# Optimization experiments

Measured on AMD Instinct MI355X. Metric: run time of the kernel, lower is better.

Reference implementation:

```python
import jax, jax.numpy as jnp
import numpy as np

B, N, K, C, NH = 2, 16384, 16, 256, 4
HD = C // NH  # head_dim = 64


def knn_gather(feat, idx):
    # feat: [B, N, D], idx: [B, N, K] -> [B, N, K, D]
    b, n, k = idx.shape
    d = feat.shape[-1]
    flat = jnp.take_along_axis(feat, idx.reshape(b, n * k)[..., None], axis=1)
    return flat.reshape(b, n, k, d)


def setup_inputs() -> dict:
    key = jax.random.key(0)
    ks = jax.random.split(key, 16)
    s_c = 1.0 / np.sqrt(C)
    s_4 = 1.0 / np.sqrt(4.0)
    s_hd = 1.0 / np.sqrt(HD)
    return {
        'h': jax.random.normal(ks[0], (B, N, C), jnp.float32),
        'P': jax.random.normal(ks[1], (B, 3, N), jnp.float32),
        'idx': jax.random.randint(ks[2], (B, N, K), 0, N),
        'Wq': jax.random.normal(ks[3], (C, C), jnp.float32) * s_c,
        'Wk': jax.random.normal(ks[4], (C, C), jnp.float32) * s_c,
        'Wv': jax.random.normal(ks[5], (C, C), jnp.float32) * s_c,
        'Wp1': jax.random.normal(ks[6], (4, C), jnp.float32) * s_4,
        'bp1': jnp.zeros((C,), jnp.float32),
        'Wp2': jax.random.normal(ks[7], (C, C), jnp.float32) * s_c,
        'bp2': jnp.zeros((C,), jnp.float32),
        'Wa1': jax.random.normal(ks[8], (HD, HD), jnp.float32) * s_hd,
        'ba1': jnp.zeros((HD,), jnp.float32),
        'Wa2': jax.random.normal(ks[9], (HD, 1), jnp.float32) * s_hd,
        'ba2': jnp.zeros((1,), jnp.float32),
        'Wo': jax.random.normal(ks[10], (C, C), jnp.float32) * s_c,
        'bo': jnp.zeros((C,), jnp.float32),
    }


def reference(h, P, idx, Wq, Wk, Wv, Wp1, bp1, Wp2, bp2, Wa1, ba1, Wa2, ba2, Wo, bo):
    b, n, c = h.shape
    P_t = jnp.swapaxes(P, 1, 2)                       # [B, N, 3]
    P_nbr = knn_gather(P_t, idx)                      # [B, N, K, 3]
    rel_pos = P_nbr - P_t[:, :, None, :]              # [B, N, K, 3]
    dist = jnp.linalg.norm(rel_pos, axis=-1, keepdims=True)
    geom = jnp.concatenate([rel_pos, dist], axis=-1)  # [B, N, K, 4]
    pe = jax.nn.relu(geom @ Wp1 + bp1) @ Wp2 + bp2    # [B, N, K, C]
    pe = pe.reshape(b, n, K, NH, HD)

    Q = (h @ Wq).reshape(b, n, 1, NH, HD)
    K_nbr = knn_gather(h @ Wk, idx).reshape(b, n, K, NH, HD)
    V_nbr = knn_gather(h @ Wv, idx).reshape(b, n, K, NH, HD)

    relation = Q - K_nbr + pe                          # [B, N, K, NH, HD]
    logits = jax.nn.relu(relation @ Wa1 + ba1) @ Wa2 + ba2  # [B, N, K, NH, 1]
    attn = jax.nn.softmax(logits, axis=2)              # softmax over K
    agg = jnp.sum(attn * (V_nbr + pe), axis=2)         # [B, N, NH, HD]
    agg = agg.reshape(b, n, c)
    return agg @ Wo + bo
```

## Files before the change

kernel.cpp:

```cpp
#include <hip/hip_runtime.h>
#include <hip/hip_bf16.h>

#define BB 2
#define NN 16384
#define KK 16
#define CC 256
#define NHH 4
#define HDD 64
#define BN (BB*NN)
#define HP 260

typedef __attribute__((ext_vector_type(8))) short short8;
typedef __attribute__((ext_vector_type(4))) short s4;
typedef __attribute__((ext_vector_type(4))) float f32x4;

__device__ __forceinline__ float bf2f(unsigned short u) {
    union { unsigned u32; float f; } x; x.u32 = ((unsigned)u) << 16; return x.f;
}
__device__ __forceinline__ unsigned short f2bf(float f) {
    union { float f; unsigned u; } x; x.f = f;
    unsigned r = x.u + 0x7FFFu + ((x.u >> 16) & 1u);
    return (unsigned short)(r >> 16);
}
__device__ __forceinline__ short8 ld8_lds(const unsigned short* p) {
    s4 lo = *(const s4*)(p);
    s4 hi = *(const s4*)(p + 4);
    short8 r;
    r[0] = lo[0]; r[1] = lo[1]; r[2] = lo[2]; r[3] = lo[3];
    r[4] = hi[0]; r[5] = hi[1]; r[6] = hi[2]; r[7] = hi[3];
    return r;
}

__global__ __launch_bounds__(256) void prep_kernel(
    const float* __restrict__ Wq, const float* __restrict__ Wk,
    const float* __restrict__ Wv, const float* __restrict__ Wp2,
    const float* __restrict__ Wo, const float* __restrict__ Wa1,
    const float* __restrict__ bp2, const float* __restrict__ ba1,
    const float* __restrict__ Wp1,
    unsigned short* WqaT, unsigned short* WkaT, unsigned short* WvT,
    unsigned short* WpeaT, unsigned short* Wp2T, unsigned short* WoT,
    float* b_u, unsigned short* Wp1aT)
{
    const int z = blockIdx.y;
    const int t = threadIdx.x;
    if (z < 3) {
        const float* W = (z == 0) ? Wq : (z == 1) ? Wk : Wp2;
        unsigned short* out = (z == 0) ? WqaT : (z == 1) ? WkaT : WpeaT;
        const int k = blockIdx.x;
        __shared__ float wrow[CC];
        __shared__ float a1[HDD * HDD];
        wrow[t] = W[k * CC + t];
        for (int i = t; i < HDD * HDD; i += 256) a1[i] = Wa1[i];
        __syncthreads();
        const int c = t;
        const int h0 = c & ~63;
        const int cl = c & 63;
        float s = 0.f;
        #pragma unroll 8
        for (int j = 0; j < HDD; ++j) s += wrow[h0 + j] * a1[j * HDD + cl];
        out[c * CC + k] = f2bf(s);
    } else if (z < 6) {
        const float* W = (z == 3) ? Wv : (z == 4) ? Wp2 : Wo;
        unsigned short* out = (z == 3) ? WvT : (z == 4) ? Wp2T : WoT;
        const int k = blockIdx.x;
        out[t * CC + k] = f2bf(W[k * CC + t]);
    } else {
        if (blockIdx.x == 0) {
            __shared__ float a1[HDD * HDD];
            for (int i = t; i < HDD * HDD; i += 256) a1[i] = Wa1[i];
            __syncthreads();
            const int c = t;
            const int h0 = c & ~63;
            const int cl = c & 63;
            float s = ba1[cl];
            #pragma unroll 8
            for (int j = 0; j < HDD; ++j) s += bp2[h0 + j] * a1[j * HDD + cl];
            b_u[c] = s;
        } else if (blockIdx.x == 1) {
            const int c = t;
            #pragma unroll
            for (int j = 0; j < 8; ++j)
                Wp1aT[c * 8 + j] = (j < 4) ? f2bf(Wp1[j * CC + c]) : (unsigned short)0;
        }
    }
}

__global__ __launch_bounds__(256) void h2bf_kernel(const float* __restrict__ h,
                                                   unsigned short* __restrict__ hbf)
{
    const int i = blockIdx.x * blockDim.x + threadIdx.x;
    const float4 v = ((const float4*)h)[i];
    ushort4 o;
    o.x = f2bf(v.x); o.y = f2bf(v.y); o.z = f2bf(v.z); o.w = f2bf(v.w);
    ((ushort4*)hbf)[i] = o;
}

template<bool FINAL>
__global__ __launch_bounds__(256) void gemm64_kernel(
    const unsigned short* __restrict__ A,
    const unsigned short* __restrict__ BT0, const unsigned short* __restrict__ BT1,
    const unsigned short* __restrict__ BT2,
    unsigned short* D0, unsigned short* D1, unsigned short* D2,
    float* Dout, const float* __restrict__ bias)
{
    const int m0 = blockIdx.x * 64;
    const unsigned short* BT;
    unsigned short* Dst = nullptr;
    if (!FINAL) {
        const int z = blockIdx.y;
        BT  = (z == 0) ? BT0 : (z == 1) ? BT1 : BT2;
        Dst = (z == 0) ? D0  : (z == 1) ? D1  : D2;
    } else {
        BT = BT0;
    }

    __shared__ __align__(16) unsigned short As[64 * 264];
    const int t = threadIdx.x;
    #pragma unroll
    for (int i = 0; i < 8; ++i) {
        const int flat = i * 2048 + t * 8;
        const int r = flat >> 8, c = flat & 255;
        short8 v = *(const short8*)(A + (size_t)(m0 + r) * CC + c);
        *(short8*)(&As[r * 264 + c]) = v;
    }
    __syncthreads();

    const int lane = t & 63, w = t >> 6;
    const int lr = lane & 15, lg = lane >> 4;

    f32x4 acc[4][4];
    #pragma unroll
    for (int mi = 0; mi < 4; ++mi)
        #pragma unroll
        for (int ni = 0; ni < 4; ++ni) acc[mi][ni] = (f32x4){0.f, 0.f, 0.f, 0.f};

    #pragma unroll
    for (int kk = 0; kk < 8; ++kk) {
        const int ko = kk * 32 + lg * 8;
        short8 a[4];
        #pragma unroll
        for (int mi = 0; mi < 4; ++mi)
            a[mi] = *(const short8*)(&As[(mi * 16 + lr) * 264 + ko]);
        #pragma unroll
        for (int ni = 0; ni < 4; ++ni) {
            const int col = w * 64 + ni * 16 + lr;
            short8 b = *(const short8*)(BT + (size_t)col * CC + ko);
            #pragma unroll
            for (int mi = 0; mi < 4; ++mi)
                acc[mi][ni] = __builtin_amdgcn_mfma_f32_16x16x32_bf16(a[mi], b, acc[mi][ni], 0, 0, 0);
        }
    }

    #pragma unroll
    for (int mi = 0; mi < 4; ++mi) {
        #pragma unroll
        for (int ni = 0; ni < 4; ++ni) {
            const int col = w * 64 + ni * 16 + lr;
            #pragma unroll
            for (int reg = 0; reg < 4; ++reg) {
                const int row = m0 + mi * 16 + lg * 4 + reg;
                const float v = acc[mi][ni][reg];
                if (FINAL) Dout[(size_t)row * CC + col] = v + bias[col];
                else       Dst[(size_t)row * CC + col] = f2bf(v);
            }
        }
    }
}

__global__ __launch_bounds__(256, 4) void fused_attn_kernel(
    const float* __restrict__ P, const int* __restrict__ idx,
    const unsigned short* __restrict__ Wp1aT, const float* __restrict__ bp1,
    const float* __restrict__ Wa2, const float* __restrict__ bp2,
    const unsigned short* __restrict__ QAbf, const unsigned short* __restrict__ KAbf,
    const unsigned short* __restrict__ Vbf,  const unsigned short* __restrict__ WpeaT,
    const unsigned short* __restrict__ Wp2T, const float* __restrict__ b_u,
    unsigned short* __restrict__ aggbf)
{
    const int pt0 = blockIdx.x * 4;
    const int b = pt0 >> 14;
    const int n0 = pt0 & (NN - 1);
    const int t = threadIdx.x;
    const int lane = t & 63, w = t >> 6;
    const int lr = lane & 15, lg = lane >> 4;

    __shared__ int nbrL[64];
    __shared__ __align__(16) unsigned short geomP[64 * 8];
    __shared__ __align__(16) unsigned short hidL[64 * HP];
    __shared__ __align__(16) unsigned short attnA[16 * 72];
    __shared__ unsigned short vbarL[16 * 72];

    const short8 zero8 = {0, 0, 0, 0, 0, 0, 0, 0};

    float qab[4][4];
    float wa2v[4], bp1v[4];
    #pragma unroll
    for (int ni = 0; ni < 4; ++ni) {
        const int c = w * 64 + ni * 16 + lr;
        wa2v[ni] = Wa2[ni * 16 + lr];
        bp1v[ni] = bp1[c];
        const float bu = b_u[c];
        #pragma unroll
        for (int mi = 0; mi < 4; ++mi)
            qab[mi][ni] = bf2f(QAbf[(size_t)(pt0 + mi) * CC + c]) + bu;
    }

    for (int i = t; i < 576; i += 256) ((unsigned*)attnA)[i] = 0;
    if (t < 64) {
        const int g = t >> 4, k = t & 15;
        const int nb = idx[(size_t)(pt0 + g) * KK + k];
        nbrL[t] = nb;
        const float* Pb = P + (size_t)b * 3 * NN;
        const int nc = n0 + g;
        const float rx = Pb[nb] - Pb[nc];
        const float ry = Pb[NN + nb] - Pb[NN + nc];
        const float rz = Pb[2 * NN + nb] - Pb[2 * NN + nc];
        const float d = sqrtf(rx * rx + ry * ry + rz * rz);
        short8 gp = {(short)f2bf(rx), (short)f2bf(ry), (short)f2bf(rz), (short)f2bf(d),
                     0, 0, 0, 0};
        *(short8*)(&geomP[t * 8]) = gp;
    }
    __syncthreads();

    {
        short8 bb[4];
        #pragma unroll
        for (int ni = 0; ni < 4; ++ni) {
            const int col = w * 64 + ni * 16 + lr;
            bb[ni] = (lg == 0) ? *(const short8*)(Wp1aT + col * 8) : zero8;
        }
        #pragma unroll
        for (int mi = 0; mi < 4; ++mi) {
            short8 ag = (lg == 0) ? *(const short8*)(&geomP[(mi * 16 + lr) * 8]) : zero8;
            #pragma unroll
            for (int ni = 0; ni < 4; ++ni) {
                f32x4 ah = (f32x4){bp1v[ni], bp1v[ni], bp1v[ni], bp1v[ni]};
                ah = __builtin_amdgcn_mfma_f32_16x16x32_bf16(ag, bb[ni], ah, 0, 0, 0);
                const int col = w * 64 + ni * 16 + lr;
                #pragma unroll
                for (int reg = 0; reg < 4; ++reg)
                    hidL[(mi * 16 + lg * 4 + reg) * HP + col] = f2bf(fmaxf(ah[reg], 0.f));
            }
        }
    }
    __syncthreads();

    f32x4 acc[4][4];
    #pragma unroll
    for (int mi = 0; mi < 4; ++mi)
        #pragma unroll
        for (int ni = 0; ni < 4; ++ni) {
            const float v = qab[mi][ni];
            acc[mi][ni] = (f32x4){v, v, v, v};
        }

    #pragma unroll
    for (int kk = 0; kk < 8; ++kk) {
        const int ko = kk * 32 + lg * 8;
        short8 a[4];
        #pragma unroll
        for (int mi = 0; mi < 4; ++mi)
            a[mi] = ld8_lds(&hidL[(mi * 16 + lr) * HP + ko]);
        #pragma unroll
        for (int ni = 0; ni < 4; ++ni) {
            const int col = w * 64 + ni * 16 + lr;
            short8 bfr = *(const short8*)(WpeaT + (size_t)col * CC + ko);
            #pragma unroll
            for (int mi = 0; mi < 4; ++mi)
                acc[mi][ni] = __builtin_amdgcn_mfma_f32_16x16x32_bf16(a[mi], bfr, acc[mi][ni], 0, 0, 0);
        }
    }

    #pragma unroll
    for (int mi = 0; mi < 4; ++mi) {
        unsigned short ka[4][4];
        #pragma unroll
        for (int reg = 0; reg < 4; ++reg) {
            const int r = mi * 16 + lg * 4 + reg;
            const size_t base = ((size_t)b * NN + nbrL[r]) * CC;
            #pragma unroll
            for (int ni = 0; ni < 4; ++ni)
                ka[reg][ni] = KAbf[base + w * 64 + ni * 16 + lr];
        }
        float pl[4];
        #pragma unroll
        for (int reg = 0; reg < 4; ++reg) {
            float s = 0.f;
            #pragma unroll
            for (int ni = 0; ni < 4; ++ni) {
                const float u = acc[mi][ni][reg] - bf2f(ka[reg][ni]);
                s += fmaxf(u, 0.f) * wa2v[ni];
            }
            s += __shfl_xor(s, 1);
            s += __shfl_xor(s, 2);
            s += __shfl_xor(s, 4);
            s += __shfl_xor(s, 8);
            pl[reg] = s;
        }
        float m = fmaxf(fmaxf(pl[0], pl[1]), fmaxf(pl[2], pl[3]));
        m = fmaxf(m, __shfl_xor(m, 16));
        m = fmaxf(m, __shfl_xor(m, 32));
        float e[4], s = 0.f;
        #pragma unroll
        for (int reg = 0; reg < 4; ++reg) { e[reg] = __expf(pl[reg] - m); s += e[reg]; }
        s += __shfl_xor(s, 16);
        s += __shfl_xor(s, 32);
        const float inv = 1.f / s;
        if (lr == 0) {
            #pragma unroll
            for (int reg = 0; reg < 4; ++reg)
                attnA[(mi * 4 + w) * 72 + mi * 16 + lg * 4 + reg] = f2bf(e[reg] * inv);
        }
    }
    __syncthreads();

    unsigned short vv[4][16];
    #pragma unroll
    for (int i = 0; i < 4; ++i) {
        const int gh = w * 4 + i;
        const int g = gh >> 2, hh = gh & 3;
        #pragma unroll
        for (int k = 0; k < 16; ++k) {
            const int r = g * 16 + k;
            vv[i][k] = Vbf[((size_t)b * NN + nbrL[r]) * CC + hh * 64 + lane];
        }
    }

    #pragma unroll
    for (int ni = 0; ni < 4; ++ni) {
        const int colAbs = w * 64 + ni * 16 + lr;
        f32x4 ab = (f32x4){0.f, 0.f, 0.f, 0.f};
        #pragma unroll
        for (int kk = 0; kk < 2; ++kk) {
            short8 aa = ld8_lds(&attnA[lr * 72 + kk * 32 + lg * 8]);
            short8 hb;
            #pragma unroll
            for (int j = 0; j < 8; ++j)
                hb[j] = (short)hidL[(kk * 32 + lg * 8 + j) * HP + colAbs];
            ab = __builtin_amdgcn_mfma_f32_16x16x32_bf16(aa, hb, ab, 0, 0, 0);
        }
        #pragma unroll
        for (int reg = 0; reg < 4; ++reg)
            hidL[(lg * 4 + reg) * HP + colAbs] = f2bf(ab[reg]);
    }

    {
        #pragma unroll
        for (int i = 0; i < 4; ++i) {
            const int gh = w * 4 + i;
            const int g = gh >> 2;
            float s = 0.f;
            #pragma unroll
            for (int k = 0; k < 16; ++k)
                s += bf2f(attnA[gh * 72 + g * 16 + k]) * bf2f(vv[i][k]);
            vbarL[gh * 72 + lane] = f2bf(s);
        }
    }
    __syncthreads();

    f32x4 acc2[4];
    #pragma unroll
    for (int ni = 0; ni < 4; ++ni) acc2[ni] = (f32x4){0.f, 0.f, 0.f, 0.f};
    #pragma unroll
    for (int kk = 0; kk < 8; ++kk) {
        const int ko = kk * 32 + lg * 8;
        short8 a = ld8_lds(&hidL[lr * HP + ko]);
        #pragma unroll
        for (int ni = 0; ni < 4; ++ni) {
            const int col = w * 64 + ni * 16 + lr;
            short8 bfr = *(const short8*)(Wp2T + (size_t)col * CC + ko);
            acc2[ni] = __builtin_amdgcn_mfma_f32_16x16x32_bf16(a, bfr, acc2[ni], 0, 0, 0);
        }
    }
    #pragma unroll
    for (int ni = 0; ni < 4; ++ni) {
        const int cl = ni * 16 + lr;
        const int c = w * 64 + cl;
        float pv;
        if      (w == 0) pv = acc2[ni][0];
        else if (w == 1) pv = acc2[ni][1];
        else if (w == 2) pv = acc2[ni][2];
        else             pv = acc2[ni][3];
        const float v = pv + bf2f(vbarL[(lg * 4 + w) * 72 + cl]) + bp2[c];
        aggbf[(size_t)(pt0 + lg) * CC + c] = f2bf(v);
    }
}

extern "C" void kernel_launch(void* const* d_in, const int* in_sizes, int n_in,
                              void* d_out, int out_size, void* d_ws, size_t ws_size,
                              hipStream_t stream)
{
    const float* h   = (const float*)d_in[0];
    const float* P   = (const float*)d_in[1];
    const int*   idx = (const int*)d_in[2];
    const float* Wq  = (const float*)d_in[3];
    const float* Wk  = (const float*)d_in[4];
    const float* Wv  = (const float*)d_in[5];
    const float* Wp1 = (const float*)d_in[6];
    const float* bp1 = (const float*)d_in[7];
    const float* Wp2 = (const float*)d_in[8];
    const float* bp2 = (const float*)d_in[9];
    const float* Wa1 = (const float*)d_in[10];
    const float* ba1 = (const float*)d_in[11];
    const float* Wa2 = (const float*)d_in[12];
    const float* Wo  = (const float*)d_in[14];
    const float* bo  = (const float*)d_in[15];

    char* ws = (char*)d_ws;
    const size_t MB16 = 16777216;
    unsigned short* WqaT  = (unsigned short*)(ws + 0);
    unsigned short* WkaT  = (unsigned short*)(ws + 131072);
    unsigned short* WvT   = (unsigned short*)(ws + 262144);
    unsigned short* WpeaT = (unsigned short*)(ws + 393216);
    unsigned short* Wp2T  = (unsigned short*)(ws + 524288);
    unsigned short* WoT   = (unsigned short*)(ws + 655360);
    float*          b_u   = (float*)(ws + 786432);
    unsigned short* Wp1aT = (unsigned short*)(ws + 787456);
    const size_t base = 1 << 20;
    unsigned short* hbf   = (unsigned short*)(ws + base + 0 * MB16);
    unsigned short* QAbf  = (unsigned short*)(ws + base + 1 * MB16);
    unsigned short* KAbf  = (unsigned short*)(ws + base + 2 * MB16);
    unsigned short* Vbf   = (unsigned short*)(ws + base + 3 * MB16);
    unsigned short* aggbf = (unsigned short*)(ws + base + 4 * MB16);
    if (ws_size < base + 5 * MB16) return;

    prep_kernel<<<dim3(256, 7), 256, 0, stream>>>(Wq, Wk, Wv, Wp2, Wo, Wa1, bp2, ba1, Wp1,
                                                  WqaT, WkaT, WvT, WpeaT, Wp2T, WoT,
                                                  b_u, Wp1aT);
    h2bf_kernel<<<BN * CC / 4 / 256, 256, 0, stream>>>(h, hbf);
    gemm64_kernel<false><<<dim3(BN / 64, 3), 256, 0, stream>>>(
        hbf, WqaT, WkaT, WvT, QAbf, KAbf, Vbf, nullptr, nullptr);
    fused_attn_kernel<<<BN / 4, 256, 0, stream>>>(P, idx, Wp1aT, bp1, Wa2, bp2,
                                                  QAbf, KAbf, Vbf, WpeaT, Wp2T, b_u, aggbf);
    gemm64_kernel<true><<<dim3(BN / 64, 1), 256, 0, stream>>>(
        aggbf, WoT, nullptr, nullptr, nullptr, nullptr, nullptr, (float*)d_out, bo);
}
```

Measured before the change: 395.8 us.

## Transpose pe MFMA so gathers are vectorized ushort4 and fold bias into Q GEMM

The positional-encoding GEMM in the attention kernel is transposed (weights as the A operand, hidden as B), so each lane holds four consecutive channels. This allows K/Q neighbour rows and V rows to be gathered as 8-byte ushort4 loads instead of scalar 2-byte loads. The softmax reduction is reorganised to match the new lane mapping. The b_u bias is now added in the Q projection GEMM epilogue rather than inside the attention kernel. The risks are a different register pressure profile and an unchanged MFMA count.

```diff
diff --git a/kernel.cpp b/kernel.cpp
--- a/kernel.cpp
+++ b/kernel.cpp
@@ -106,8 +106,9 @@
     const int m0 = blockIdx.x * 64;
     const unsigned short* BT;
     unsigned short* Dst = nullptr;
+    int z = 0;
     if (!FINAL) {
-        const int z = blockIdx.y;
+        z = blockIdx.y;
         BT  = (z == 0) ? BT0 : (z == 1) ? BT1 : BT2;
         Dst = (z == 0) ? D0  : (z == 1) ? D1  : D2;
     } else {
@@ -156,12 +157,13 @@
         #pragma unroll
         for (int ni = 0; ni < 4; ++ni) {
             const int col = w * 64 + ni * 16 + lr;
+            const float bc = (FINAL || z == 0) ? bias[col] : 0.f;
             #pragma unroll
             for (int reg = 0; reg < 4; ++reg) {
                 const int row = m0 + mi * 16 + lg * 4 + reg;
                 const float v = acc[mi][ni][reg];
                 if (FINAL) Dout[(size_t)row * CC + col] = v + bias[col];
-                else       Dst[(size_t)row * CC + col] = f2bf(v);
+                else       Dst[(size_t)row * CC + col] = f2bf(v + bc);
             }
         }
     }
@@ -173,7 +175,7 @@
     const float* __restrict__ Wa2, const float* __restrict__ bp2,
     const unsigned short* __restrict__ QAbf, const unsigned short* __restrict__ KAbf,
     const unsigned short* __restrict__ Vbf,  const unsigned short* __restrict__ WpeaT,
-    const unsigned short* __restrict__ Wp2T, const float* __restrict__ b_u,
+    const unsigned short* __restrict__ Wp2T,
     unsigned short* __restrict__ aggbf)
 {
     const int pt0 = blockIdx.x * 4;
@@ -191,18 +193,9 @@
 
     const short8 zero8 = {0, 0, 0, 0, 0, 0, 0, 0};
 
-    float qab[4][4];
-    float wa2v[4], bp1v[4];
-    #pragma unroll
-    for (int ni = 0; ni < 4; ++ni) {
-        const int c = w * 64 + ni * 16 + lr;
-        wa2v[ni] = Wa2[ni * 16 + lr];
-        bp1v[ni] = bp1[c];
-        const float bu = b_u[c];
-        #pragma unroll
-        for (int mi = 0; mi < 4; ++mi)
-            qab[mi][ni] = bf2f(QAbf[(size_t)(pt0 + mi) * CC + c]) + bu;
-    }
+    float bp1v[4];
+    #pragma unroll
+    for (int ni = 0; ni < 4; ++ni) bp1v[ni] = bp1[w * 64 + ni * 16 + lr];
 
     for (int i = t; i < 576; i += 256) ((unsigned*)attnA)[i] = 0;
     if (t < 64) {
@@ -244,86 +237,88 @@
     }
     __syncthreads();
 
-    f32x4 acc[4][4];
-    #pragma unroll
-    for (int mi = 0; mi < 4; ++mi)
-        #pragma unroll
-        for (int ni = 0; ni < 4; ++ni) {
-            const float v = qab[mi][ni];
-            acc[mi][ni] = (f32x4){v, v, v, v};
-        }
-
-    #pragma unroll
-    for (int kk = 0; kk < 8; ++kk) {
-        const int ko = kk * 32 + lg * 8;
-        short8 a[4];
-        #pragma unroll
-        for (int mi = 0; mi < 4; ++mi)
-            a[mi] = ld8_lds(&hidL[(mi * 16 + lr) * HP + ko]);
-        #pragma unroll
-        for (int ni = 0; ni < 4; ++ni) {
-            const int col = w * 64 + ni * 16 + lr;
-            short8 bfr = *(const short8*)(WpeaT + (size_t)col * CC + ko);
-            #pragma unroll
-            for (int mi = 0; mi < 4; ++mi)
-                acc[mi][ni] = __builtin_amdgcn_mfma_f32_16x16x32_bf16(a[mi], bfr, acc[mi][ni], 0, 0, 0);
-        }
-    }
-
-    #pragma unroll
-    for (int mi = 0; mi < 4; ++mi) {
-        unsigned short ka[4][4];
-        #pragma unroll
-        for (int reg = 0; reg < 4; ++reg) {
-            const int r = mi * 16 + lg * 4 + reg;
-            const size_t base = ((size_t)b * NN + nbrL[r]) * CC;
-            #pragma unroll
-            for (int ni = 0; ni < 4; ++ni)
-                ka[reg][ni] = KAbf[base + w * 64 + ni * 16 + lr];
-        }
-        float pl[4];
-        #pragma unroll
-        for (int reg = 0; reg < 4; ++reg) {
-            float s = 0.f;
-            #pragma unroll
-            for (int ni = 0; ni < 4; ++ni) {
-                const float u = acc[mi][ni][reg] - bf2f(ka[reg][ni]);
-                s += fmaxf(u, 0.f) * wa2v[ni];
+    const size_t bNN = (size_t)b * NN;
+    int nb4[4];
+    #pragma unroll
+    for (int RB = 0; RB < 4; ++RB) nb4[RB] = nbrL[RB * 16 + lr];
+
+    f32x4 slog[4];
+    #pragma unroll
+    for (int RB = 0; RB < 4; ++RB) slog[RB] = (f32x4){0.f, 0.f, 0.f, 0.f};
+
+    #pragma unroll
+    for (int pair = 0; pair < 2; ++pair) {
+        ushort4 kaP[2][4], qaP[2][4];
+        #pragma unroll
+        for (int cbi = 0; cbi < 2; ++cbi) {
+            const int CB = pair * 2 + cbi;
+            const int cb0 = w * 64 + CB * 16 + lg * 4;
+            #pragma unroll
+            for (int RB = 0; RB < 4; ++RB) {
+                kaP[cbi][RB] = *(const ushort4*)(KAbf + (bNN + nb4[RB]) * CC + cb0);
+                qaP[cbi][RB] = *(const ushort4*)(QAbf + (size_t)(pt0 + RB) * CC + cb0);
             }
-            s += __shfl_xor(s, 1);
-            s += __shfl_xor(s, 2);
-            s += __shfl_xor(s, 4);
-            s += __shfl_xor(s, 8);
-            pl[reg] = s;
-        }
-        float m = fmaxf(fmaxf(pl[0], pl[1]), fmaxf(pl[2], pl[3]));
-        m = fmaxf(m, __shfl_xor(m, 16));
-        m = fmaxf(m, __shfl_xor(m, 32));
-        float e[4], s = 0.f;
-        #pragma unroll
-        for (int reg = 0; reg < 4; ++reg) { e[reg] = __expf(pl[reg] - m); s += e[reg]; }
+        }
+
+        f32x4 acc8[2][4];
+        #pragma unroll
+        for (int cbi = 0; cbi < 2; ++cbi)
+            #pragma unroll
+            for (int RB = 0; RB < 4; ++RB) acc8[cbi][RB] = (f32x4){0.f, 0.f, 0.f, 0.f};
+
+        #pragma unroll
+        for (int kk = 0; kk < 8; ++kk) {
+            const int ko = kk * 32 + lg * 8;
+            short8 aw0 = *(const short8*)(WpeaT + (size_t)(w * 64 + (pair * 2 + 0) * 16 + lr) * CC + ko);
+            short8 aw1 = *(const short8*)(WpeaT + (size_t)(w * 64 + (pair * 2 + 1) * 16 + lr) * CC + ko);
+            #pragma unroll
+            for (int RB = 0; RB < 4; ++RB) {
+                short8 bh = ld8_lds(&hidL[(RB * 16 + lr) * HP + ko]);
+                acc8[0][RB] = __builtin_amdgcn_mfma_f32_16x16x32_bf16(aw0, bh, acc8[0][RB], 0, 0, 0);
+                acc8[1][RB] = __builtin_amdgcn_mfma_f32_16x16x32_bf16(aw1, bh, acc8[1][RB], 0, 0, 0);
+            }
+        }
+
+        #pragma unroll
+        for (int cbi = 0; cbi < 2; ++cbi) {
+            const int CB = pair * 2 + cbi;
+            const float4 w4 = *(const float4*)(Wa2 + CB * 16 + lg * 4);
+            #pragma unroll
+            for (int RB = 0; RB < 4; ++RB) {
+                const ushort4 ka4 = kaP[cbi][RB], qa4 = qaP[cbi][RB];
+                slog[RB][0] += fmaxf(acc8[cbi][RB][0] + bf2f(qa4.x) - bf2f(ka4.x), 0.f) * w4.x;
+                slog[RB][1] += fmaxf(acc8[cbi][RB][1] + bf2f(qa4.y) - bf2f(ka4.y), 0.f) * w4.y;
+                slog[RB][2] += fmaxf(acc8[cbi][RB][2] + bf2f(qa4.z) - bf2f(ka4.z), 0.f) * w4.z;
+                slog[RB][3] += fmaxf(acc8[cbi][RB][3] + bf2f(qa4.w) - bf2f(ka4.w), 0.f) * w4.w;
+            }
+        }
+    }
+
+    #pragma unroll
+    for (int RB = 0; RB < 4; ++RB) {
+        float s = slog[RB][0] + slog[RB][1] + slog[RB][2] + slog[RB][3];
         s += __shfl_xor(s, 16);
         s += __shfl_xor(s, 32);
-        const float inv = 1.f / s;
-        if (lr == 0) {
-            #pragma unroll
-            for (int reg = 0; reg < 4; ++reg)
-                attnA[(mi * 4 + w) * 72 + mi * 16 + lg * 4 + reg] = f2bf(e[reg] * inv);
-        }
+        float m = s;
+        m = fmaxf(m, __shfl_xor(m, 1));
+        m = fmaxf(m, __shfl_xor(m, 2));
+        m = fmaxf(m, __shfl_xor(m, 4));
+        m = fmaxf(m, __shfl_xor(m, 8));
+        const float e = __expf(s - m);
+        float d = e;
+        d += __shfl_xor(d, 1);
+        d += __shfl_xor(d, 2);
+        d += __shfl_xor(d, 4);
+        d += __shfl_xor(d, 8);
+        if (lg == 0)
+            attnA[(RB * 4 + w) * 72 + RB * 16 + lr] = f2bf(e / d);
     }
     __syncthreads();
 
-    unsigned short vv[4][16];
-    #pragma unroll
-    for (int i = 0; i < 4; ++i) {
-        const int gh = w * 4 + i;
-        const int g = gh >> 2, hh = gh & 3;
-        #pragma unroll
-        for (int k = 0; k < 16; ++k) {
-            const int r = g * 16 + k;
-            vv[i][k] = Vbf[((size_t)b * NN + nbrL[r]) * CC + hh * 64 + lane];
-        }
-    }
+    ushort4 vv[16];
+    #pragma unroll
+    for (int k = 0; k < 16; ++k)
+        vv[k] = *(const ushort4*)(Vbf + (bNN + nbrL[w * 16 + k]) * CC + lane * 4);
 
     #pragma unroll
     for (int ni = 0; ni < 4; ++ni) {
@@ -344,16 +339,20 @@
     }
 
     {
-        #pragma unroll
-        for (int i = 0; i < 4; ++i) {
-            const int gh = w * 4 + i;
-            const int g = gh >> 2;
-            float s = 0.f;
-            #pragma unroll
-            for (int k = 0; k < 16; ++k)
-                s += bf2f(attnA[gh * 72 + g * 16 + k]) * bf2f(vv[i][k]);
-            vbarL[gh * 72 + lane] = f2bf(s);
-        }
+        const int hh = lane >> 4;
+        const int dbase = (lane & 15) * 4;
+        float s0 = 0.f, s1 = 0.f, s2 = 0.f, s3 = 0.f;
+        #pragma unroll
+        for (int k = 0; k < 16; ++k) {
+            const float at = bf2f(attnA[(w * 4 + hh) * 72 + w * 16 + k]);
+            s0 += at * bf2f((unsigned short)vv[k].x);
+            s1 += at * bf2f((unsigned short)vv[k].y);
+            s2 += at * bf2f((unsigned short)vv[k].z);
+            s3 += at * bf2f((unsigned short)vv[k].w);
+        }
+        ushort4 o;
+        o.x = f2bf(s0); o.y = f2bf(s1); o.z = f2bf(s2); o.w = f2bf(s3);
+        *(ushort4*)(&vbarL[(w * 4 + hh) * 72 + dbase]) = o;
     }
     __syncthreads();
 
@@ -428,9 +427,9 @@
                                                   b_u, Wp1aT);
     h2bf_kernel<<<BN * CC / 4 / 256, 256, 0, stream>>>(h, hbf);
     gemm64_kernel<false><<<dim3(BN / 64, 3), 256, 0, stream>>>(
-        hbf, WqaT, WkaT, WvT, QAbf, KAbf, Vbf, nullptr, nullptr);
+        hbf, WqaT, WkaT, WvT, QAbf, KAbf, Vbf, nullptr, b_u);
     fused_attn_kernel<<<BN / 4, 256, 0, stream>>>(P, idx, Wp1aT, bp1, Wa2, bp2,
-                                                  QAbf, KAbf, Vbf, WpeaT, Wp2T, b_u, aggbf);
+                                                  QAbf, KAbf, Vbf, WpeaT, Wp2T, aggbf);
     gemm64_kernel<true><<<dim3(BN / 64, 1), 256, 0, stream>>>(
         aggbf, WoT, nullptr, nullptr, nullptr, nullptr, nullptr, (float*)d_out, bo);
 }
```

Result: slower. 420.0 us (+6.1%).

## Fold query bias into GEMM, per-wave geometry MFMA, vectorized V gather

Applied to the files above, without the earlier changes.

The b_u bias is now added in the QKV GEMM epilogue for the Q output, so the attention kernel no longer loads and adds it. Each wave now computes the geometry features for its own point in registers and runs the first position-encoding MFMA directly, which removes the geomP LDS staging buffer and one block barrier. The V neighbour gather now loads ushort4 vectors per lane instead of scalar shorts, and the attention-weighted V sum works on four channels per lane. Launch bounds drop from 4 to 3 blocks per CU, which gives the compiler more registers but may lower occupancy.

```diff
diff --git a/kernel.cpp b/kernel.cpp
--- a/kernel.cpp
+++ b/kernel.cpp
@@ -106,8 +106,9 @@
     const int m0 = blockIdx.x * 64;
     const unsigned short* BT;
     unsigned short* Dst = nullptr;
+    int z = 0;
     if (!FINAL) {
-        const int z = blockIdx.y;
+        z = blockIdx.y;
         BT  = (z == 0) ? BT0 : (z == 1) ? BT1 : BT2;
         Dst = (z == 0) ? D0  : (z == 1) ? D1  : D2;
     } else {
@@ -156,24 +157,25 @@
         #pragma unroll
         for (int ni = 0; ni < 4; ++ni) {
             const int col = w * 64 + ni * 16 + lr;
+            const float bc = (FINAL || z == 0) ? bias[col] : 0.f;
             #pragma unroll
             for (int reg = 0; reg < 4; ++reg) {
                 const int row = m0 + mi * 16 + lg * 4 + reg;
                 const float v = acc[mi][ni][reg];
                 if (FINAL) Dout[(size_t)row * CC + col] = v + bias[col];
-                else       Dst[(size_t)row * CC + col] = f2bf(v);
+                else       Dst[(size_t)row * CC + col] = f2bf(v + bc);
             }
         }
     }
 }
 
-__global__ __launch_bounds__(256, 4) void fused_attn_kernel(
+__global__ __launch_bounds__(256, 3) void fused_attn_kernel(
     const float* __restrict__ P, const int* __restrict__ idx,
     const unsigned short* __restrict__ Wp1aT, const float* __restrict__ bp1,
     const float* __restrict__ Wa2, const float* __restrict__ bp2,
     const unsigned short* __restrict__ QAbf, const unsigned short* __restrict__ KAbf,
     const unsigned short* __restrict__ Vbf,  const unsigned short* __restrict__ WpeaT,
-    const unsigned short* __restrict__ Wp2T, const float* __restrict__ b_u,
+    const unsigned short* __restrict__ Wp2T,
     unsigned short* __restrict__ aggbf)
 {
     const int pt0 = blockIdx.x * 4;
@@ -184,7 +186,6 @@
     const int lr = lane & 15, lg = lane >> 4;
 
     __shared__ int nbrL[64];
-    __shared__ __align__(16) unsigned short geomP[64 * 8];
     __shared__ __align__(16) unsigned short hidL[64 * HP];
     __shared__ __align__(16) unsigned short attnA[16 * 72];
     __shared__ unsigned short vbarL[16 * 72];
@@ -192,55 +193,43 @@
     const short8 zero8 = {0, 0, 0, 0, 0, 0, 0, 0};
 
     float qab[4][4];
-    float wa2v[4], bp1v[4];
+    float wa2v[4];
     #pragma unroll
     for (int ni = 0; ni < 4; ++ni) {
         const int c = w * 64 + ni * 16 + lr;
         wa2v[ni] = Wa2[ni * 16 + lr];
-        bp1v[ni] = bp1[c];
-        const float bu = b_u[c];
         #pragma unroll
         for (int mi = 0; mi < 4; ++mi)
-            qab[mi][ni] = bf2f(QAbf[(size_t)(pt0 + mi) * CC + c]) + bu;
+            qab[mi][ni] = bf2f(QAbf[(size_t)(pt0 + mi) * CC + c]);
     }
 
     for (int i = t; i < 576; i += 256) ((unsigned*)attnA)[i] = 0;
-    if (t < 64) {
-        const int g = t >> 4, k = t & 15;
-        const int nb = idx[(size_t)(pt0 + g) * KK + k];
-        nbrL[t] = nb;
+
+    float rx = 0.f, ry = 0.f, rz = 0.f, dd = 0.f;
+    if (lane < 16) {
+        const int nb_ = idx[(size_t)(pt0 + w) * KK + lane];
+        nbrL[w * 16 + lane] = nb_;
         const float* Pb = P + (size_t)b * 3 * NN;
-        const int nc = n0 + g;
-        const float rx = Pb[nb] - Pb[nc];
-        const float ry = Pb[NN + nb] - Pb[NN + nc];
-        const float rz = Pb[2 * NN + nb] - Pb[2 * NN + nc];
-        const float d = sqrtf(rx * rx + ry * ry + rz * rz);
-        short8 gp = {(short)f2bf(rx), (short)f2bf(ry), (short)f2bf(rz), (short)f2bf(d),
-                     0, 0, 0, 0};
-        *(short8*)(&geomP[t * 8]) = gp;
-    }
-    __syncthreads();
-
-    {
-        short8 bb[4];
-        #pragma unroll
-        for (int ni = 0; ni < 4; ++ni) {
-            const int col = w * 64 + ni * 16 + lr;
-            bb[ni] = (lg == 0) ? *(const short8*)(Wp1aT + col * 8) : zero8;
-        }
-        #pragma unroll
-        for (int mi = 0; mi < 4; ++mi) {
-            short8 ag = (lg == 0) ? *(const short8*)(&geomP[(mi * 16 + lr) * 8]) : zero8;
-            #pragma unroll
-            for (int ni = 0; ni < 4; ++ni) {
-                f32x4 ah = (f32x4){bp1v[ni], bp1v[ni], bp1v[ni], bp1v[ni]};
-                ah = __builtin_amdgcn_mfma_f32_16x16x32_bf16(ag, bb[ni], ah, 0, 0, 0);
-                const int col = w * 64 + ni * 16 + lr;
-                #pragma unroll
-                for (int reg = 0; reg < 4; ++reg)
-                    hidL[(mi * 16 + lg * 4 + reg) * HP + col] = f2bf(fmaxf(ah[reg], 0.f));
-            }
-        }
+        const int nc = n0 + w;
+        rx = Pb[nb_] - Pb[nc];
+        ry = Pb[NN + nb_] - Pb[NN + nc];
+        rz = Pb[2 * NN + nb_] - Pb[2 * NN + nc];
+        dd = sqrtf(rx * rx + ry * ry + rz * rz);
+    }
+    short8 ag = zero8;
+    if (lane < 16) {
+        ag[0] = (short)f2bf(rx); ag[1] = (short)f2bf(ry);
+        ag[2] = (short)f2bf(rz); ag[3] = (short)f2bf(dd);
+    }
+    #pragma unroll
+    for (int nb = 0; nb < 16; ++nb) {
+        short8 bb = (lg == 0) ? *(const short8*)(Wp1aT + (nb * 16 + lr) * 8) : zero8;
+        const float bp = bp1[nb * 16 + lr];
+        f32x4 ah = (f32x4){bp, bp, bp, bp};
+        ah = __builtin_amdgcn_mfma_f32_16x16x32_bf16(ag, bb, ah, 0, 0, 0);
+        #pragma unroll
+        for (int reg = 0; reg < 4; ++reg)
+            hidL[(w * 16 + lg * 4 + reg) * HP + nb * 16 + lr] = f2bf(fmaxf(ah[reg], 0.f));
     }
     __syncthreads();
 
@@ -313,17 +302,11 @@
     }
     __syncthreads();
 
-    unsigned short vv[4][16];
-    #pragma unroll
-    for (int i = 0; i < 4; ++i) {
-        const int gh = w * 4 + i;
-        const int g = gh >> 2, hh = gh & 3;
-        #pragma unroll
-        for (int k = 0; k < 16; ++k) {
-            const int r = g * 16 + k;
-            vv[i][k] = Vbf[((size_t)b * NN + nbrL[r]) * CC + hh * 64 + lane];
-        }
-    }
+    const size_t bNN = (size_t)b * NN;
+    ushort4 vv[16];
+    #pragma unroll
+    for (int k = 0; k < 16; ++k)
+        vv[k] = *(const ushort4*)(Vbf + (bNN + nbrL[w * 16 + k]) * CC + lane * 4);
 
     #pragma unroll
     for (int ni = 0; ni < 4; ++ni) {
@@ -344,16 +327,20 @@
     }
 
     {
-        #pragma unroll
-        for (int i = 0; i < 4; ++i) {
-            const int gh = w * 4 + i;
-            const int g = gh >> 2;
-            float s = 0.f;
-            #pragma unroll
-            for (int k = 0; k < 16; ++k)
-                s += bf2f(attnA[gh * 72 + g * 16 + k]) * bf2f(vv[i][k]);
-            vbarL[gh * 72 + lane] = f2bf(s);
-        }
+        const int hh = lane >> 4;
+        const int dbase = (lane & 15) * 4;
+        float s0 = 0.f, s1 = 0.f, s2 = 0.f, s3 = 0.f;
+        #pragma unroll
+        for (int k = 0; k < 16; ++k) {
+            const float at = bf2f(attnA[(w * 4 + hh) * 72 + w * 16 + k]);
+            s0 += at * bf2f((unsigned short)vv[k].x);
+            s1 += at * bf2f((unsigned short)vv[k].y);
+            s2 += at * bf2f((unsigned short)vv[k].z);
+            s3 += at * bf2f((unsigned short)vv[k].w);
+        }
+        ushort4 o;
+        o.x = f2bf(s0); o.y = f2bf(s1); o.z = f2bf(s2); o.w = f2bf(s3);
+        *(ushort4*)(&vbarL[(w * 4 + hh) * 72 + dbase]) = o;
     }
     __syncthreads();
 
@@ -428,9 +415,9 @@
                                                   b_u, Wp1aT);
     h2bf_kernel<<<BN * CC / 4 / 256, 256, 0, stream>>>(h, hbf);
     gemm64_kernel<false><<<dim3(BN / 64, 3), 256, 0, stream>>>(
-        hbf, WqaT, WkaT, WvT, QAbf, KAbf, Vbf, nullptr, nullptr);
+        hbf, WqaT, WkaT, WvT, QAbf, KAbf, Vbf, nullptr, b_u);
     fused_attn_kernel<<<BN / 4, 256, 0, stream>>>(P, idx, Wp1aT, bp1, Wa2, bp2,
-                                                  QAbf, KAbf, Vbf, WpeaT, Wp2T, b_u, aggbf);
+                                                  QAbf, KAbf, Vbf, WpeaT, Wp2T, aggbf);
     gemm64_kernel<true><<<dim3(BN / 64, 1), 256, 0, stream>>>(
         aggbf, WoT, nullptr, nullptr, nullptr, nullptr, nullptr, (float*)d_out, bo);
 }
```

Result: slower. 442.0 us (+11.7%).

## Prefetch K neighbor gathers early, fold Q bias into GEMM, use lightweight barriers

Applied to the files above, without the earlier changes.

Moves the gather of neighbor K rows to just after the first barrier so it overlaps the positional-encoding MFMA work instead of stalling inside the softmax loop. The V gathers are now issued before the barrier that precedes the attention-weighted reduction. The b_u bias is added in the QKV GEMM epilogue rather than per point in the fused kernel, and __syncthreads is replaced by a custom s_waitcnt lgkmcnt(0) plus s_barrier macro. Launch bounds drop from 4 to 3 blocks per SM to make room for the extra prefetch registers. This trades occupancy for latency hiding, and the custom barrier may weaken ordering guarantees.

```diff
diff --git a/kernel.cpp b/kernel.cpp
--- a/kernel.cpp
+++ b/kernel.cpp
@@ -13,6 +13,13 @@
 typedef __attribute__((ext_vector_type(8))) short short8;
 typedef __attribute__((ext_vector_type(4))) short s4;
 typedef __attribute__((ext_vector_type(4))) float f32x4;
+
+#define WAVE_BARRIER() do {                                      \
+    __builtin_amdgcn_sched_barrier(0);                           \
+    asm volatile("s_waitcnt lgkmcnt(0)" ::: "memory");           \
+    __builtin_amdgcn_s_barrier();                                \
+    __builtin_amdgcn_sched_barrier(0);                           \
+} while (0)
 
 __device__ __forceinline__ float bf2f(unsigned short u) {
     union { unsigned u32; float f; } x; x.u32 = ((unsigned)u) << 16; return x.f;
@@ -106,8 +113,9 @@
     const int m0 = blockIdx.x * 64;
     const unsigned short* BT;
     unsigned short* Dst = nullptr;
+    int z = 0;
     if (!FINAL) {
-        const int z = blockIdx.y;
+        z = blockIdx.y;
         BT  = (z == 0) ? BT0 : (z == 1) ? BT1 : BT2;
         Dst = (z == 0) ? D0  : (z == 1) ? D1  : D2;
     } else {
@@ -156,24 +164,25 @@
         #pragma unroll
         for (int ni = 0; ni < 4; ++ni) {
             const int col = w * 64 + ni * 16 + lr;
+            const float bc = (FINAL || z == 0) ? bias[col] : 0.f;
             #pragma unroll
             for (int reg = 0; reg < 4; ++reg) {
                 const int row = m0 + mi * 16 + lg * 4 + reg;
                 const float v = acc[mi][ni][reg];
                 if (FINAL) Dout[(size_t)row * CC + col] = v + bias[col];
-                else       Dst[(size_t)row * CC + col] = f2bf(v);
+                else       Dst[(size_t)row * CC + col] = f2bf(v + bc);
             }
         }
     }
 }
 
-__global__ __launch_bounds__(256, 4) void fused_attn_kernel(
+__global__ __launch_bounds__(256, 3) void fused_attn_kernel(
     const float* __restrict__ P, const int* __restrict__ idx,
     const unsigned short* __restrict__ Wp1aT, const float* __restrict__ bp1,
     const float* __restrict__ Wa2, const float* __restrict__ bp2,
     const unsigned short* __restrict__ QAbf, const unsigned short* __restrict__ KAbf,
     const unsigned short* __restrict__ Vbf,  const unsigned short* __restrict__ WpeaT,
-    const unsigned short* __restrict__ Wp2T, const float* __restrict__ b_u,
+    const unsigned short* __restrict__ Wp2T,
     unsigned short* __restrict__ aggbf)
 {
     const int pt0 = blockIdx.x * 4;
@@ -191,17 +200,15 @@
 
     const short8 zero8 = {0, 0, 0, 0, 0, 0, 0, 0};
 
-    float qab[4][4];
-    float wa2v[4], bp1v[4];
+    float wa2v[4], bp1v[4], qab[4][4];
     #pragma unroll
     for (int ni = 0; ni < 4; ++ni) {
         const int c = w * 64 + ni * 16 + lr;
         wa2v[ni] = Wa2[ni * 16 + lr];
         bp1v[ni] = bp1[c];
-        const float bu = b_u[c];
         #pragma unroll
         for (int mi = 0; mi < 4; ++mi)
-            qab[mi][ni] = bf2f(QAbf[(size_t)(pt0 + mi) * CC + c]) + bu;
+            qab[mi][ni] = bf2f(QAbf[(size_t)(pt0 + mi) * CC + c]);
     }
 
     for (int i = t; i < 576; i += 256) ((unsigned*)attnA)[i] = 0;
@@ -219,7 +226,19 @@
                      0, 0, 0, 0};
         *(short8*)(&geomP[t * 8]) = gp;
     }
-    __syncthreads();
+    WAVE_BARRIER();
+
+    unsigned short ka[4][4][4];
+    #pragma unroll
+    for (int mi = 0; mi < 4; ++mi)
+        #pragma unroll
+        for (int reg = 0; reg < 4; ++reg) {
+            const int r = mi * 16 + lg * 4 + reg;
+            const size_t base = ((size_t)b * NN + nbrL[r]) * CC;
+            #pragma unroll
+            for (int ni = 0; ni < 4; ++ni)
+                ka[mi][reg][ni] = KAbf[base + w * 64 + ni * 16 + lr];
+        }
 
     {
         short8 bb[4];
@@ -242,7 +261,7 @@
             }
         }
     }
-    __syncthreads();
+    WAVE_BARRIER();
 
     f32x4 acc[4][4];
     #pragma unroll
@@ -272,22 +291,13 @@
 
     #pragma unroll
     for (int mi = 0; mi < 4; ++mi) {
-        unsigned short ka[4][4];
-        #pragma unroll
-        for (int reg = 0; reg < 4; ++reg) {
-            const int r = mi * 16 + lg * 4 + reg;
-            const size_t base = ((size_t)b * NN + nbrL[r]) * CC;
-            #pragma unroll
-            for (int ni = 0; ni < 4; ++ni)
-                ka[reg][ni] = KAbf[base + w * 64 + ni * 16 + lr];
-        }
         float pl[4];
         #pragma unroll
         for (int reg = 0; reg < 4; ++reg) {
             float s = 0.f;
             #pragma unroll
             for (int ni = 0; ni < 4; ++ni) {
-                const float u = acc[mi][ni][reg] - bf2f(ka[reg][ni]);
+                const float u = acc[mi][ni][reg] - bf2f(ka[mi][reg][ni]);
                 s += fmaxf(u, 0.f) * wa2v[ni];
             }
             s += __shfl_xor(s, 1);
@@ -311,8 +321,8 @@
                 attnA[(mi * 4 + w) * 72 + mi * 16 + lg * 4 + reg] = f2bf(e[reg] * inv);
         }
     }
-    __syncthreads();
-
+
+    const size_t bNN = (size_t)b * NN;
     unsigned short vv[4][16];
     #pragma unroll
     for (int i = 0; i < 4; ++i) {
@@ -321,9 +331,10 @@
         #pragma unroll
         for (int k = 0; k < 16; ++k) {
             const int r = g * 16 + k;
-            vv[i][k] = Vbf[((size_t)b * NN + nbrL[r]) * CC + hh * 64 + lane];
-        }
-    }
+            vv[i][k] = Vbf[(bNN + nbrL[r]) * CC + hh * 64 + lane];
+        }
+    }
+    WAVE_BARRIER();
 
     #pragma unroll
     for (int ni = 0; ni < 4; ++ni) {
@@ -355,7 +366,7 @@
             vbarL[gh * 72 + lane] = f2bf(s);
         }
     }
-    __syncthreads();
+    WAVE_BARRIER();
 
     f32x4 acc2[4];
     #pragma unroll
@@ -428,9 +439,9 @@
                                                   b_u, Wp1aT);
     h2bf_kernel<<<BN * CC / 4 / 256, 256, 0, stream>>>(h, hbf);
     gemm64_kernel<false><<<dim3(BN / 64, 3), 256, 0, stream>>>(
-        hbf, WqaT, WkaT, WvT, QAbf, KAbf, Vbf, nullptr, nullptr);
+        hbf, WqaT, WkaT, WvT, QAbf, KAbf, Vbf, nullptr, b_u);
     fused_attn_kernel<<<BN / 4, 256, 0, stream>>>(P, idx, Wp1aT, bp1, Wa2, bp2,
-                                                  QAbf, KAbf, Vbf, WpeaT, Wp2T, b_u, aggbf);
+                                                  QAbf, KAbf, Vbf, WpeaT, Wp2T, aggbf);
     gemm64_kernel<true><<<dim3(BN / 64, 1), 256, 0, stream>>>(
         aggbf, WoT, nullptr, nullptr, nullptr, nullptr, nullptr, (float*)d_out, bo);
 }
```

New measurement: 616.0 us. +55.6%, slower.
